# Performance work log

Hardware: AMD Instinct MI355X
Metric: run time of the kernel (lower is better)

## Reference

```python
import jax, jax.numpy as jnp
import numpy as np

BATCH, SEQ, EMBED, HIDDEN, VOCAB = 32, 64, 512, 512, 32000

def setup_inputs() -> dict:
    key = jax.random.key(0)
    ks = jax.random.split(key, 11)
    s = lambda k, shape, scale: jax.random.normal(k, shape, dtype=jnp.float32) * scale
    return {
        "features": s(ks[0], (BATCH, HIDDEN), 1.0),
        "captions": jax.random.randint(ks[1], (BATCH, SEQ), 0, VOCAB),
        "embedding": s(ks[2], (VOCAB, EMBED), 1.0),
        "Wz_w": s(ks[3], (HIDDEN, EMBED + HIDDEN), 0.03),
        "Wz_b": s(ks[4], (HIDDEN,), 0.03),
        "Wr_w": s(ks[5], (HIDDEN, EMBED + HIDDEN), 0.03),
        "Wr_b": s(ks[6], (HIDDEN,), 0.03),
        "Wh_w": s(ks[7], (HIDDEN, EMBED + HIDDEN), 0.03),
        "Wh_b": s(ks[8], (HIDDEN,), 0.03),
        "fc_w": s(ks[9], (VOCAB, HIDDEN), 0.03),
        "fc_b": s(ks[10], (VOCAB,), 0.03),
    }

def reference(features, captions, embedding, Wz_w, Wz_b, Wr_w, Wr_b, Wh_w, Wh_b, fc_w, fc_b):
    # embeddings: [B, T, E] -> scan over time with xs [T, B, E]
    emb = embedding[captions]                      # [B, T, E]
    xs = jnp.swapaxes(emb, 0, 1)                   # [T, B, E]

    def step(h, x_t):
        comb = jnp.concatenate([x_t, h], axis=1)                   # [B, E+H]
        z = jax.nn.sigmoid(comb @ Wz_w.T + Wz_b)                   # update gate
        r = jax.nn.sigmoid(comb @ Wr_w.T + Wr_b)                   # reset gate
        comb_r = jnp.concatenate([x_t, r * h], axis=1)
        h_tilde = jnp.tanh(comb_r @ Wh_w.T + Wh_b)
        h_new = (1.0 - z) * h + z * h_tilde
        return h_new, h_new

    _, hs = jax.lax.scan(step, features, xs)       # hs: [T, B, H]
    hs = jnp.swapaxes(hs, 0, 1)                    # [B, T, H]
    # output projection done once over all timesteps (same math as per-step fc_out)
    logits = jnp.einsum('bth,vh->btv', hs, fc_w) + fc_b  # [B, T, V]
    return logits
```

## Files before the change

kernel.cpp:

```cpp
#include <hip/hip_runtime.h>
#include <hip/hip_bf16.h>

typedef __bf16 bf16;
typedef __bf16 bf16x8 __attribute__((ext_vector_type(8)));
typedef float f32x4 __attribute__((ext_vector_type(4)));
typedef unsigned int u32x4 __attribute__((ext_vector_type(4)));

#define B_SZ 32
#define T_SZ 64
#define H_SZ 512
#define V_SZ 32000
#define NWG_REC 8
#define NWRK 500
#define MTILES 16

__device__ __forceinline__ float sigmoidf_(float v) { return 1.0f / (1.0f + expf(-v)); }

__device__ __forceinline__ bf16x8 cvt8(const float* __restrict__ p) {
  float4 a = *(const float4*)p;
  float4 b = *(const float4*)(p + 4);
  bf16x8 o;
  o[0] = (bf16)a.x; o[1] = (bf16)a.y; o[2] = (bf16)a.z; o[3] = (bf16)a.w;
  o[4] = (bf16)b.x; o[5] = (bf16)b.y; o[6] = (bf16)b.z; o[7] = (bf16)b.w;
  return o;
}

#define GLD(dst, base, off) \
  asm volatile("global_load_dwordx4 %0, %1, off offset:" off " sc0 sc1" \
               : "=v"(dst) : "v"(base))
#define LOADALL(af, base) do { \
  GLD(af[0],  base, "0");   GLD(af[1],  base, "64");  GLD(af[2],  base, "128"); GLD(af[3],  base, "192"); \
  GLD(af[4],  base, "256"); GLD(af[5],  base, "320"); GLD(af[6],  base, "384"); GLD(af[7],  base, "448"); \
  GLD(af[8],  base, "512"); GLD(af[9],  base, "576"); GLD(af[10], base, "640"); GLD(af[11], base, "704"); \
  GLD(af[12], base, "768"); GLD(af[13], base, "832"); GLD(af[14], base, "896"); GLD(af[15], base, "960"); \
} while (0)
#define GST2(base, off, val) do { \
  unsigned int w_ = (unsigned int)__builtin_bit_cast(unsigned short, (bf16)(val)); \
  asm volatile("global_store_short %0, %1, off offset:" off " sc0 sc1" \
               :: "v"(base), "v"(w_) : "memory"); \
} while (0)
#define WAITV  asm volatile("s_waitcnt vmcnt(0)" ::: "memory")
#define SCHEDB __builtin_amdgcn_sched_barrier(0)

__device__ __forceinline__ int llc_poll(const int* p) {
  int r;
  asm volatile("global_load_dword %0, %1, off sc0 sc1\n\ts_waitcnt vmcnt(0)"
               : "=v"(r) : "v"(p) : "memory");
  return r;
}

__global__ __launch_bounds__(256) void xproj_k(
    const int* __restrict__ caps, const float* __restrict__ emb,
    const float* __restrict__ B0, const float* __restrict__ B1, const float* __restrict__ B2,
    const float* __restrict__ bias0, const float* __restrict__ bias1, const float* __restrict__ bias2,
    float* __restrict__ C, int prep_start,
    const float* __restrict__ feat, bf16* __restrict__ h_g, int* __restrict__ ctr,
    bf16* __restrict__ whp_dst)
{
  __shared__ __align__(16) bf16 lA[128 * 32];
  __shared__ __align__(16) bf16 lB[128 * 32];
  const int tid = threadIdx.x;
  const int bidx = blockIdx.x;

  if (bidx >= prep_start) {
    int i = (bidx - prep_start) * 256 + tid;
    int w = i >> 15;
    int rem = i & 32767;
    int n = rem >> 6;
    int k8 = (rem & 63) * 8;
    const float* W = (w == 0) ? B0 : (w == 1) ? B1 : B2;
    *(bf16x8*)(whp_dst + (long)w * 262144 + n * 512 + k8) = cvt8(W + (long)n * 1024 + 512 + k8);
    if (i < B_SZ * H_SZ) h_g[i] = (bf16)feat[i];
    if (i < 128) ctr[i] = 0;
    return;
  }

  const int lane = tid & 63;
  const int l15  = lane & 15;
  const int kb8  = (lane >> 4) * 8;
  const int wid  = tid >> 6;
  const int wm   = wid >> 1, wn = wid & 1;
  const int mtile = bidx % 16, ntile = bidx / 16;
  const int m0 = mtile * 128, n0 = ntile * 128;

  int wsel = n0 >> 9;
  const float* Bv   = wsel == 0 ? B0 : wsel == 1 ? B1 : B2;
  const float* bias = wsel == 0 ? bias0 : wsel == 1 ? bias1 : bias2;
  int nb = n0 & 511;

  f32x4 acc[4][4] = {};

  for (int k0 = 0; k0 < 512; k0 += 32) {
    #pragma unroll
    for (int j = 0; j < 2; ++j) {
      int c = j * 256 + tid;
      int row = c >> 2;
      int kc = (c & 3) * 8;
      *(bf16x8*)&lA[row * 32 + kc] = cvt8(emb + (long)caps[m0 + row] * 512 + k0 + kc);
      *(bf16x8*)&lB[row * 32 + kc] = cvt8(Bv + (long)(nb + row) * 1024 + k0 + kc);
    }
    __syncthreads();
    bf16x8 af[4], bfr[4];
    #pragma unroll
    for (int mf = 0; mf < 4; ++mf)
      af[mf] = *(const bf16x8*)&lA[(wm * 64 + mf * 16 + l15) * 32 + kb8];
    #pragma unroll
    for (int nf = 0; nf < 4; ++nf)
      bfr[nf] = *(const bf16x8*)&lB[(wn * 64 + nf * 16 + l15) * 32 + kb8];
    #pragma unroll
    for (int mf = 0; mf < 4; ++mf)
      #pragma unroll
      for (int nf = 0; nf < 4; ++nf)
        acc[mf][nf] = __builtin_amdgcn_mfma_f32_16x16x32_bf16(af[mf], bfr[nf], acc[mf][nf], 0, 0, 0);
    __syncthreads();
  }

  #pragma unroll
  for (int mf = 0; mf < 4; ++mf)
    #pragma unroll
    for (int nf = 0; nf < 4; ++nf)
      #pragma unroll
      for (int r = 0; r < 4; ++r) {
        int row = m0 + wm * 64 + mf * 16 + (lane >> 4) * 4 + r;
        int lc  = wn * 64 + nf * 16 + l15;
        C[(long)row * 1536 + n0 + lc] = acc[mf][nf][r] + bias[nb + lc];
      }
}

__global__ __launch_bounds__(512, 2) void fused_k(
    const float* __restrict__ X,
    const bf16* __restrict__ Wzh, const bf16* __restrict__ Wrh, const bf16* __restrict__ Whh,
    const float* __restrict__ feat,
    bf16* __restrict__ h_g, bf16* __restrict__ rh_g,
    bf16* __restrict__ hs, int* __restrict__ ctr,
    const float* __restrict__ fcw, const float* __restrict__ fc_b, float* __restrict__ out)
{
  __shared__ __align__(16) char smem[65536];
  const int tid  = threadIdx.x;
  const int bid  = blockIdx.x;
  const int lane = tid & 63;
  const int l15  = lane & 15;
  const int q    = lane >> 4;
  int* prog = ctr + 64;

  if (bid < NWG_REC) {
    char* ldsb = smem;
    const int u    = bid * 8 + (tid >> 6);
    const int kb   = q * 8;
    const int rq   = q * 4;
    const int b0   = (u >> 5) * 16;
    const int gcol = (u & 31) * 16 + l15;

    u32x4 Bz[16], Br[16];
    LOADALL(Bz, Wzh + (long)gcol * 512 + kb);
    LOADALL(Br, Wrh + (long)gcol * 512 + kb);
    WAITV;
    const bf16* whb = Whh + (long)gcol * 512 + kb;

    float hprev[4];
    #pragma unroll
    for (int r = 0; r < 4; ++r) hprev[r] = feat[(b0 + rq + r) * 512 + gcol];

    const float* xb = X + (long)(b0 + rq) * 64 * 1536 + gcol;
    float xz[4], xr[4];
    #pragma unroll
    for (int r = 0; r < 4; ++r) {
      xz[r] = xb[r * 98304];
      xr[r] = xb[r * 98304 + 512];
    }

    const int srow0 = tid >> 6;
    const int soff0 = (tid * 16) ^ ((srow0 & 7) << 4);
    const int soff1 = (8192 + tid * 16) ^ ((srow0 & 7) << 4);
    const int fbase = (l15 * 1024 + q * 16) ^ ((l15 & 7) << 4);

    bf16* rhst = rh_g + (b0 + rq) * 512 + gcol;
    bf16* hst  = h_g  + (b0 + rq) * 512 + gcol;

    int epoch = 0;
    for (int t = 0; t < T_SZ; ++t) {
      {
        const bf16* src = h_g + b0 * 512;
        u32x4 v0, v1;
        GLD(v0, src + tid * 8, "0");
        GLD(v1, src + 4096 + tid * 8, "0");
        WAITV;
        SCHEDB;
        *(u32x4*)(ldsb + soff0) = v0;
        *(u32x4*)(ldsb + soff1) = v1;
      }
      __syncthreads();
      f32x4 ze = {}, re = {};
      #pragma unroll
      for (int kk = 0; kk < 16; ++kk) {
        bf16x8 a = *(const bf16x8*)(ldsb + (fbase ^ (kk * 64)));
        ze = __builtin_amdgcn_mfma_f32_16x16x32_bf16(a, __builtin_bit_cast(bf16x8, Bz[kk]), ze, 0, 0, 0);
        re = __builtin_amdgcn_mfma_f32_16x16x32_bf16(a, __builtin_bit_cast(bf16x8, Br[kk]), re, 0, 0, 0);
      }
      {
        float r0 = sigmoidf_(re[0] + xr[0]) * hprev[0];
        float r1 = sigmoidf_(re[1] + xr[1]) * hprev[1];
        float r2 = sigmoidf_(re[2] + xr[2]) * hprev[2];
        float r3 = sigmoidf_(re[3] + xr[3]) * hprev[3];
        GST2(rhst, "0", r0); GST2(rhst, "1024", r1); GST2(rhst, "2048", r2); GST2(rhst, "3072", r3);
      }
      ++epoch;
      WAITV;
      __syncthreads();
      if (tid == 0)
        __hip_atomic_fetch_add(ctr, 1, __ATOMIC_RELAXED, __HIP_MEMORY_SCOPE_AGENT);
      f32x4 zf;
      #pragma unroll
      for (int r = 0; r < 4; ++r) zf[r] = sigmoidf_(ze[r] + xz[r]);
      float xh[4];
      #pragma unroll
      for (int r = 0; r < 4; ++r) xh[r] = xb[r * 98304 + t * 1536 + 1024];
      if (tid == 0) {
        while (__hip_atomic_load(ctr, __ATOMIC_RELAXED, __HIP_MEMORY_SCOPE_AGENT) < NWG_REC * epoch)
          __builtin_amdgcn_s_sleep(1);
      }
      __syncthreads();

      {
        const bf16* src = rh_g + b0 * 512;
        u32x4 v0, v1;
        GLD(v0, src + tid * 8, "0");
        GLD(v1, src + 4096 + tid * 8, "0");
        WAITV;
        SCHEDB;
        *(u32x4*)(ldsb + soff0) = v0;
        *(u32x4*)(ldsb + soff1) = v1;
      }
      __syncthreads();
      f32x4 he = {};
      #pragma unroll
      for (int kk = 0; kk < 16; ++kk) {
        bf16x8 a = *(const bf16x8*)(ldsb + (fbase ^ (kk * 64)));
        u32x4 bh = *(const u32x4*)(whb + kk * 32);
        he = __builtin_amdgcn_mfma_f32_16x16x32_bf16(a, __builtin_bit_cast(bf16x8, bh), he, 0, 0, 0);
      }
      bf16* ph = hs + (long)(t * 32 + b0 + rq) * 512 + gcol;
      #pragma unroll
      for (int r = 0; r < 4; ++r) {
        float ht = tanhf(he[r] + xh[r]);
        float hn = hprev[r] + zf[r] * (ht - hprev[r]);
        hprev[r] = hn;
      }
      GST2(hst, "0", hprev[0]); GST2(hst, "1024", hprev[1]);
      GST2(hst, "2048", hprev[2]); GST2(hst, "3072", hprev[3]);
      GST2(ph, "0", hprev[0]); GST2(ph, "1024", hprev[1]);
      GST2(ph, "2048", hprev[2]); GST2(ph, "3072", hprev[3]);
      ++epoch;
      WAITV;
      __syncthreads();
      if (tid == 0)
        __hip_atomic_fetch_add(ctr, 1, __ATOMIC_RELAXED, __HIP_MEMORY_SCOPE_AGENT);
      if (t + 1 < T_SZ) {
        #pragma unroll
        for (int r = 0; r < 4; ++r) {
          xz[r] = xb[r * 98304 + (t + 1) * 1536];
          xr[r] = xb[r * 98304 + (t + 1) * 1536 + 512];
        }
      }
      if (tid == 0) {
        while (__hip_atomic_load(ctr, __ATOMIC_RELAXED, __HIP_MEMORY_SCOPE_AGENT) < NWG_REC * epoch)
          __builtin_amdgcn_s_sleep(1);
        if (bid == 0) {
          int e = epoch;
          asm volatile("global_store_dword %0, %1, off sc0 sc1" :: "v"(prog), "v"(e) : "memory");
        }
      }
      __syncthreads();
    }
    return;
  }

  const int n0 = (bid - NWG_REC) * 64;
  bf16* lB = (bf16*)smem;

  #pragma unroll
  for (int i = 0; i < 8; ++i) {
    int c = i * 512 + tid;
    int L = c * 16;
    int j = L >> 10;
    int k0 = (L & 1023) >> 1;
    bf16x8 v = cvt8(fcw + (long)(n0 + j) * 512 + k0);
    *(bf16x8*)((char*)lB + (L ^ ((j & 7) << 4))) = v;
  }
  __syncthreads();

  const int wid = tid >> 6;
  const int kb  = q * 8;
  int fbB[4];
  #pragma unroll
  for (int nf = 0; nf < 4; ++nf) {
    int j = nf * 16 + l15;
    fbB[nf] = ((j << 10) + q * 16) ^ ((l15 & 7) << 4);
  }
  float bias_v[4];
  #pragma unroll
  for (int nf = 0; nf < 4; ++nf) bias_v[nf] = fc_b[n0 + nf * 16 + l15];

  for (int m = 0; m < MTILES; ++m) {
    if (tid == 0) {
      const int tgt = 8 * (m + 1);
      while (llc_poll(prog) < tgt) __builtin_amdgcn_s_sleep(32);
    }
    __syncthreads();

    u32x4 af[16];
    LOADALL(af, hs + (long)(m * 128 + wid * 16 + l15) * 512 + kb);
    WAITV;
    SCHEDB;
    f32x4 acc[4] = {};
    #pragma unroll
    for (int kk = 0; kk < 16; ++kk) {
      bf16x8 a = __builtin_bit_cast(bf16x8, af[kk]);
      #pragma unroll
      for (int nf = 0; nf < 4; ++nf) {
        bf16x8 b = *(const bf16x8*)((char*)lB + (fbB[nf] ^ (kk * 64)));
        acc[nf] = __builtin_amdgcn_mfma_f32_16x16x32_bf16(a, b, acc[nf], 0, 0, 0);
      }
    }
    #pragma unroll
    for (int nf = 0; nf < 4; ++nf)
      #pragma unroll
      for (int r = 0; r < 4; ++r) {
        int rr = m * 128 + wid * 16 + q * 4 + r;
        int tt = rr >> 5, b = rr & 31;
        out[(long)(b * 64 + tt) * 32000 + n0 + nf * 16 + l15] = acc[nf][r] + bias_v[nf];
      }
  }
}

extern "C" void kernel_launch(void* const* d_in, const int* in_sizes, int n_in,
                              void* d_out, int out_size, void* d_ws, size_t ws_size,
                              hipStream_t stream) {
  const float* feat = (const float*)d_in[0];
  const int*   caps = (const int*)d_in[1];
  const float* emb  = (const float*)d_in[2];
  const float* Wz_w = (const float*)d_in[3];
  const float* Wz_b = (const float*)d_in[4];
  const float* Wr_w = (const float*)d_in[5];
  const float* Wr_b = (const float*)d_in[6];
  const float* Wh_w = (const float*)d_in[7];
  const float* Wh_b = (const float*)d_in[8];
  const float* fc_w = (const float*)d_in[9];
  const float* fc_b = (const float*)d_in[10];
  float* out = (float*)d_out;

  char* ws = (char*)d_ws;
  float* X_all = (float*)(ws + 0);
  bf16*  h_g   = (bf16*) (ws + 12582912);
  bf16*  rh_g  = (bf16*) (ws + 12615680);
  bf16*  hs    = (bf16*) (ws + 12648448);
  bf16*  Whp   = (bf16*) (ws + 14745600);
  int*   ctr   = (int*)  (ws + 16318464);

  xproj_k<<<dim3(576), dim3(256), 0, stream>>>(
      caps, emb, Wz_w, Wr_w, Wh_w, Wz_b, Wr_b, Wh_b, X_all, 192,
      feat, h_g, ctr, Whp);

  fused_k<<<dim3(NWG_REC + NWRK), dim3(512), 0, stream>>>(
      X_all, Whp, Whp + 262144, Whp + 524288, feat, h_g, rh_g, hs, ctr,
      fc_w, fc_b, out);
}
```

Measured before the change: 690.2 us.

## Split recurrent barrier into two independent batch groups and keep Wh in registers

The recurrent workgroups are split into two groups of four, one per 16-row batch half, each with its own counter and progress flag. This replaces the eight-workgroup global barrier with a smaller per-group one. The Wh weights are now preloaded into registers instead of being reloaded every step, and h is read straight from the hs history buffer (slot t), which removes the separate h_g store. The FC workers poll both progress flags, and raw asm loads are replaced by plain loads. In exchange, register pressure rises from holding three weight fragments per lane.

```diff
diff --git a/kernel.cpp b/kernel.cpp
--- a/kernel.cpp
+++ b/kernel.cpp
@@ -28,12 +28,6 @@
 #define GLD(dst, base, off) \
   asm volatile("global_load_dwordx4 %0, %1, off offset:" off " sc0 sc1" \
                : "=v"(dst) : "v"(base))
-#define LOADALL(af, base) do { \
-  GLD(af[0],  base, "0");   GLD(af[1],  base, "64");  GLD(af[2],  base, "128"); GLD(af[3],  base, "192"); \
-  GLD(af[4],  base, "256"); GLD(af[5],  base, "320"); GLD(af[6],  base, "384"); GLD(af[7],  base, "448"); \
-  GLD(af[8],  base, "512"); GLD(af[9],  base, "576"); GLD(af[10], base, "640"); GLD(af[11], base, "704"); \
-  GLD(af[12], base, "768"); GLD(af[13], base, "832"); GLD(af[14], base, "896"); GLD(af[15], base, "960"); \
-} while (0)
 #define GST2(base, off, val) do { \
   unsigned int w_ = (unsigned int)__builtin_bit_cast(unsigned short, (bf16)(val)); \
   asm volatile("global_store_short %0, %1, off offset:" off " sc0 sc1" \
@@ -54,7 +48,7 @@
     const float* __restrict__ B0, const float* __restrict__ B1, const float* __restrict__ B2,
     const float* __restrict__ bias0, const float* __restrict__ bias1, const float* __restrict__ bias2,
     float* __restrict__ C, int prep_start,
-    const float* __restrict__ feat, bf16* __restrict__ h_g, int* __restrict__ ctr,
+    const float* __restrict__ feat, bf16* __restrict__ hs, int* __restrict__ ctr,
     bf16* __restrict__ whp_dst)
 {
   __shared__ __align__(16) bf16 lA[128 * 32];
@@ -70,7 +64,7 @@
     int k8 = (rem & 63) * 8;
     const float* W = (w == 0) ? B0 : (w == 1) ? B1 : B2;
     *(bf16x8*)(whp_dst + (long)w * 262144 + n * 512 + k8) = cvt8(W + (long)n * 1024 + 512 + k8);
-    if (i < B_SZ * H_SZ) h_g[i] = (bf16)feat[i];
+    if (i < B_SZ * H_SZ) hs[i] = (bf16)feat[i];
     if (i < 128) ctr[i] = 0;
     return;
   }
@@ -131,8 +125,7 @@
     const float* __restrict__ X,
     const bf16* __restrict__ Wzh, const bf16* __restrict__ Wrh, const bf16* __restrict__ Whh,
     const float* __restrict__ feat,
-    bf16* __restrict__ h_g, bf16* __restrict__ rh_g,
-    bf16* __restrict__ hs, int* __restrict__ ctr,
+    bf16* __restrict__ rh_g, bf16* __restrict__ hs, int* __restrict__ ctr,
     const float* __restrict__ fcw, const float* __restrict__ fc_b, float* __restrict__ out)
 {
   __shared__ __align__(16) char smem[65536];
@@ -141,7 +134,6 @@
   const int lane = tid & 63;
   const int l15  = lane & 15;
   const int q    = lane >> 4;
-  int* prog = ctr + 64;
 
   if (bid < NWG_REC) {
     char* ldsb = smem;
@@ -150,12 +142,20 @@
     const int rq   = q * 4;
     const int b0   = (u >> 5) * 16;
     const int gcol = (u & 31) * 16 + l15;
-
-    u32x4 Bz[16], Br[16];
-    LOADALL(Bz, Wzh + (long)gcol * 512 + kb);
-    LOADALL(Br, Wrh + (long)gcol * 512 + kb);
-    WAITV;
-    const bf16* whb = Whh + (long)gcol * 512 + kb;
+    const int grp  = bid >> 2;
+    int* mctr  = ctr + grp * 32;
+    int* progG = ctr + 64 + grp * 32;
+
+    u32x4 Bz[16], Br[16], Bh[16];
+    #pragma unroll
+    for (int kk = 0; kk < 16; ++kk) {
+      Bz[kk] = *(const u32x4*)(Wzh + (long)gcol * 512 + kk * 32 + kb);
+      Br[kk] = *(const u32x4*)(Wrh + (long)gcol * 512 + kk * 32 + kb);
+      Bh[kk] = *(const u32x4*)(Whh + (long)gcol * 512 + kk * 32 + kb);
+    }
+    #pragma unroll
+    for (int kk = 0; kk < 16; ++kk)
+      asm volatile("" : "+v"(Bz[kk]), "+v"(Br[kk]), "+v"(Bh[kk]));
 
     float hprev[4];
     #pragma unroll
@@ -175,12 +175,11 @@
     const int fbase = (l15 * 1024 + q * 16) ^ ((l15 & 7) << 4);
 
     bf16* rhst = rh_g + (b0 + rq) * 512 + gcol;
-    bf16* hst  = h_g  + (b0 + rq) * 512 + gcol;
 
     int epoch = 0;
     for (int t = 0; t < T_SZ; ++t) {
       {
-        const bf16* src = h_g + b0 * 512;
+        const bf16* src = hs + (long)(t * 32 + b0) * 512;
         u32x4 v0, v1;
         GLD(v0, src + tid * 8, "0");
         GLD(v1, src + 4096 + tid * 8, "0");
@@ -197,26 +196,25 @@
         ze = __builtin_amdgcn_mfma_f32_16x16x32_bf16(a, __builtin_bit_cast(bf16x8, Bz[kk]), ze, 0, 0, 0);
         re = __builtin_amdgcn_mfma_f32_16x16x32_bf16(a, __builtin_bit_cast(bf16x8, Br[kk]), re, 0, 0, 0);
       }
+      float xh[4];
+      #pragma unroll
+      for (int r = 0; r < 4; ++r) xh[r] = xb[r * 98304 + t * 1536 + 1024];
+      f32x4 zf;
       {
         float r0 = sigmoidf_(re[0] + xr[0]) * hprev[0];
         float r1 = sigmoidf_(re[1] + xr[1]) * hprev[1];
         float r2 = sigmoidf_(re[2] + xr[2]) * hprev[2];
         float r3 = sigmoidf_(re[3] + xr[3]) * hprev[3];
         GST2(rhst, "0", r0); GST2(rhst, "1024", r1); GST2(rhst, "2048", r2); GST2(rhst, "3072", r3);
+        #pragma unroll
+        for (int r = 0; r < 4; ++r) zf[r] = sigmoidf_(ze[r] + xz[r]);
       }
       ++epoch;
       WAITV;
       __syncthreads();
-      if (tid == 0)
-        __hip_atomic_fetch_add(ctr, 1, __ATOMIC_RELAXED, __HIP_MEMORY_SCOPE_AGENT);
-      f32x4 zf;
-      #pragma unroll
-      for (int r = 0; r < 4; ++r) zf[r] = sigmoidf_(ze[r] + xz[r]);
-      float xh[4];
-      #pragma unroll
-      for (int r = 0; r < 4; ++r) xh[r] = xb[r * 98304 + t * 1536 + 1024];
       if (tid == 0) {
-        while (__hip_atomic_load(ctr, __ATOMIC_RELAXED, __HIP_MEMORY_SCOPE_AGENT) < NWG_REC * epoch)
+        __hip_atomic_fetch_add(mctr, 1, __ATOMIC_RELAXED, __HIP_MEMORY_SCOPE_AGENT);
+        while (__hip_atomic_load(mctr, __ATOMIC_RELAXED, __HIP_MEMORY_SCOPE_AGENT) < 4 * epoch)
           __builtin_amdgcn_s_sleep(1);
       }
       __syncthreads();
@@ -236,25 +234,8 @@
       #pragma unroll
       for (int kk = 0; kk < 16; ++kk) {
         bf16x8 a = *(const bf16x8*)(ldsb + (fbase ^ (kk * 64)));
-        u32x4 bh = *(const u32x4*)(whb + kk * 32);
-        he = __builtin_amdgcn_mfma_f32_16x16x32_bf16(a, __builtin_bit_cast(bf16x8, bh), he, 0, 0, 0);
-      }
-      bf16* ph = hs + (long)(t * 32 + b0 + rq) * 512 + gcol;
-      #pragma unroll
-      for (int r = 0; r < 4; ++r) {
-        float ht = tanhf(he[r] + xh[r]);
-        float hn = hprev[r] + zf[r] * (ht - hprev[r]);
-        hprev[r] = hn;
-      }
-      GST2(hst, "0", hprev[0]); GST2(hst, "1024", hprev[1]);
-      GST2(hst, "2048", hprev[2]); GST2(hst, "3072", hprev[3]);
-      GST2(ph, "0", hprev[0]); GST2(ph, "1024", hprev[1]);
-      GST2(ph, "2048", hprev[2]); GST2(ph, "3072", hprev[3]);
-      ++epoch;
-      WAITV;
-      __syncthreads();
-      if (tid == 0)
-        __hip_atomic_fetch_add(ctr, 1, __ATOMIC_RELAXED, __HIP_MEMORY_SCOPE_AGENT);
+        he = __builtin_amdgcn_mfma_f32_16x16x32_bf16(a, __builtin_bit_cast(bf16x8, Bh[kk]), he, 0, 0, 0);
+      }
       if (t + 1 < T_SZ) {
         #pragma unroll
         for (int r = 0; r < 4; ++r) {
@@ -262,12 +243,25 @@
           xr[r] = xb[r * 98304 + (t + 1) * 1536 + 512];
         }
       }
+      bf16* ph = hs + (long)((t + 1) * 32 + b0 + rq) * 512 + gcol;
+      #pragma unroll
+      for (int r = 0; r < 4; ++r) {
+        float ht = tanhf(he[r] + xh[r]);
+        float hn = hprev[r] + zf[r] * (ht - hprev[r]);
+        hprev[r] = hn;
+      }
+      GST2(ph, "0", hprev[0]); GST2(ph, "1024", hprev[1]);
+      GST2(ph, "2048", hprev[2]); GST2(ph, "3072", hprev[3]);
+      ++epoch;
+      WAITV;
+      __syncthreads();
       if (tid == 0) {
-        while (__hip_atomic_load(ctr, __ATOMIC_RELAXED, __HIP_MEMORY_SCOPE_AGENT) < NWG_REC * epoch)
+        __hip_atomic_fetch_add(mctr, 1, __ATOMIC_RELAXED, __HIP_MEMORY_SCOPE_AGENT);
+        while (__hip_atomic_load(mctr, __ATOMIC_RELAXED, __HIP_MEMORY_SCOPE_AGENT) < 4 * epoch)
           __builtin_amdgcn_s_sleep(1);
-        if (bid == 0) {
+        if ((bid & 3) == 0) {
           int e = epoch;
-          asm volatile("global_store_dword %0, %1, off sc0 sc1" :: "v"(prog), "v"(e) : "memory");
+          asm volatile("global_store_dword %0, %1, off sc0 sc1" :: "v"(progG), "v"(e) : "memory");
         }
       }
       __syncthreads();
@@ -291,6 +285,7 @@
 
   const int wid = tid >> 6;
   const int kb  = q * 8;
+  const bf16* hsW = hs + 16384;
   int fbB[4];
   #pragma unroll
   for (int nf = 0; nf < 4; ++nf) {
@@ -302,16 +297,17 @@
   for (int nf = 0; nf < 4; ++nf) bias_v[nf] = fc_b[n0 + nf * 16 + l15];
 
   for (int m = 0; m < MTILES; ++m) {
-    if (tid == 0) {
+    if (tid < 2) {
       const int tgt = 8 * (m + 1);
-      while (llc_poll(prog) < tgt) __builtin_amdgcn_s_sleep(32);
+      const int* p = ctr + 64 + tid * 32;
+      while (llc_poll(p) < tgt) __builtin_amdgcn_s_sleep(32);
     }
     __syncthreads();
 
+    const bf16* abase = hsW + (long)(m * 128 + wid * 16 + l15) * 512 + kb;
     u32x4 af[16];
-    LOADALL(af, hs + (long)(m * 128 + wid * 16 + l15) * 512 + kb);
-    WAITV;
-    SCHEDB;
+    #pragma unroll
+    for (int kk = 0; kk < 16; ++kk) af[kk] = *(const u32x4*)(abase + kk * 32);
     f32x4 acc[4] = {};
     #pragma unroll
     for (int kk = 0; kk < 16; ++kk) {
@@ -351,17 +347,16 @@
 
   char* ws = (char*)d_ws;
   float* X_all = (float*)(ws + 0);
-  bf16*  h_g   = (bf16*) (ws + 12582912);
-  bf16*  rh_g  = (bf16*) (ws + 12615680);
-  bf16*  hs    = (bf16*) (ws + 12648448);
+  bf16*  rh_g  = (bf16*) (ws + 12582912);
+  bf16*  hs    = (bf16*) (ws + 12615680);
   bf16*  Whp   = (bf16*) (ws + 14745600);
   int*   ctr   = (int*)  (ws + 16318464);
 
   xproj_k<<<dim3(576), dim3(256), 0, stream>>>(
       caps, emb, Wz_w, Wr_w, Wh_w, Wz_b, Wr_b, Wh_b, X_all, 192,
-      feat, h_g, ctr, Whp);
+      feat, hs, ctr, Whp);
 
   fused_k<<<dim3(NWG_REC + NWRK), dim3(512), 0, stream>>>(
-      X_all, Whp, Whp + 262144, Whp + 524288, feat, h_g, rh_g, hs, ctr,
+      X_all, Whp, Whp + 262144, Whp + 524288, feat, rh_g, hs, ctr,
       fc_w, fc_b, out);
 }
```

New measurement: 633.6 us. -8.2%, faster.
